# Performance work log

Hardware: AMD Instinct MI355X
Metric: run time of the kernel (lower is better)

Reference implementation:

```python
import jax, jax.numpy as jnp
import numpy as np

B, T, F = 4096, 256, 20
VOCAB, EMB = 1281, 4
UNITS = (64, 32, 32, 32)


def setup_inputs() -> dict:
    key = jax.random.key(0)
    ks = jax.random.split(key, 16)
    feats = jax.random.normal(ks[0], (B, T, F), jnp.float32)
    ids = jax.random.randint(ks[1], (B, T), 0, VOCAB).astype(jnp.float32)
    input_tensor = feats.at[:, :, 1].set(ids)  # column 1 = org ids
    W_emb = jax.random.normal(ks[2], (VOCAB, EMB), jnp.float32) * 0.1
    in_dims = (F - 2 + 1 + EMB,) + UNITS[:-1]  # (23, 64, 32, 32)
    out = {"input_tensor": input_tensor, "W_emb": W_emb}
    for i, (din, u) in enumerate(zip(in_dims, UNITS)):
        out[f"k{i}"] = jax.random.normal(ks[3 + 3 * i], (din, 3 * u), jnp.float32) * 0.1
        out[f"rk{i}"] = jax.random.normal(ks[4 + 3 * i], (u, 3 * u), jnp.float32) * 0.1
        out[f"b{i}"] = jnp.zeros((2, 3 * u), jnp.float32)  # [input_bias, recurrent_bias] (reset_after)
    out["Wd"] = jax.random.normal(ks[15], (UNITS[-1], 2), jnp.float32) * 0.1
    out["bd"] = jnp.zeros((2,), jnp.float32)
    return out


def _gru(h, x, k, rk, b):
    # Keras GRUCell, reset_after=True (TF2 default)
    mx = x @ k + b[0]
    mh = h @ rk + b[1]
    xz, xr, xh = jnp.split(mx, 3, axis=-1)
    hz, hr, hh = jnp.split(mh, 3, axis=-1)
    z = jax.nn.sigmoid(xz + hz)
    r = jax.nn.sigmoid(xr + hr)
    hc = jnp.tanh(xh + r * hh)
    return z * h + (1.0 - z) * hc


def reference(input_tensor, W_emb, k0, rk0, b0, k1, rk1, b1, k2, rk2, b2, k3, rk3, b3, Wd, bd):
    f0 = input_tensor[:, :, :1]                      # [B,T,1]
    ids = input_tensor[:, :, 1].astype(jnp.int32)    # [B,T]
    rest = input_tensor[:, :, 2:]                    # [B,T,F-2]
    emb = W_emb[ids]                                 # [B,T,EMB]
    x = jnp.concatenate([f0, rest, emb], axis=-1)    # [B,T,F+3]
    xs = jnp.swapaxes(x, 0, 1)                       # [T,B,F+3]
    bsz = x.shape[0]
    h_init = tuple(jnp.zeros((bsz, u), x.dtype) for u in UNITS)
    layer_params = ((k0, rk0, b0), (k1, rk1, b1), (k2, rk2, b2), (k3, rk3, b3))

    def step(carry, xt):
        hs = []
        inp = xt
        for h, (k, rk, b) in zip(carry, layer_params):
            h = _gru(h, inp, k, rk, b)
            hs.append(h)
            inp = h
        return tuple(hs), None

    hs, _ = jax.lax.scan(step, h_init, xs)
    # return_sequences + [:, -1, :] == final hidden state of last layer
    logits = hs[-1] @ Wd + bd
    return jax.nn.softmax(logits, axis=-1)
```

## Files before the change

### kernel.cpp

```cpp
#include <hip/hip_runtime.h>


typedef __attribute__((ext_vector_type(8))) __bf16 bf16x8;
typedef __attribute__((ext_vector_type(4))) float f32x4;

#define TT 256
#define FF 20
#define BT 16
#define CH 64
#define SH0 72
#define SH1 40
#define XSTR 648
#define NTHR 768
#define LOG2E 1.44269504f

__device__ __forceinline__ f32x4 mfma16(bf16x8 a, bf16x8 b, f32x4 c) {
  return __builtin_amdgcn_mfma_f32_16x16x32_bf16(a, b, c, 0, 0, 0);
}

__device__ __forceinline__ bf16x8 bfragW(const float* W, int Kreal, int N,
                                         int ncol, int kbase) {
  bf16x8 r;
#pragma unroll
  for (int j = 0; j < 8; ++j) {
    int k = kbase + j;
    r[j] = (__bf16)(k < Kreal ? W[k * N + ncol] : 0.f);
  }
  return r;
}

extern "C" __global__ void __launch_bounds__(NTHR, 3)
gru4(const float* __restrict__ inp, const float* __restrict__ Wemb,
     const float* __restrict__ k0, const float* __restrict__ rk0, const float* __restrict__ b0,
     const float* __restrict__ k1, const float* __restrict__ rk1, const float* __restrict__ b1,
     const float* __restrict__ k2, const float* __restrict__ rk2, const float* __restrict__ b2,
     const float* __restrict__ k3, const float* __restrict__ rk3, const float* __restrict__ b3,
     const float* __restrict__ Wd, const float* __restrict__ bd,
     float* __restrict__ out)
{
  __shared__ __align__(16) __bf16 x_ch[CH * XSTR];
  __shared__ __align__(16) __bf16 h0_lds[2][BT * SH0];
  __shared__ __align__(16) __bf16 h1_lds[2][BT * SH1];
  __shared__ __align__(16) __bf16 h2_lds[2][BT * SH1];
  __shared__ __align__(16) __bf16 h3_lds[2][BT * SH1];
  __shared__ __align__(16) float h3f[BT * 32];

  const int tid  = threadIdx.x;
  const int lane = tid & 63;
  const int w    = tid >> 6;
  const int col  = lane & 15;
  const int kb   = (lane >> 4) * 8;
  const int rowq = (lane >> 4) * 4;
  const long bbase = (long)blockIdx.x * BT;
  const float* binp = inp + bbase * TT * FF;

  bf16x8 zf;
#pragma unroll
  for (int j = 0; j < 8; ++j) zf[j] = (__bf16)0.f;

  bf16x8 WzP = zf, WrP = zf, WgP = zf;
  bf16x8 WzX = zf, WrX = zf, WgX = zf;
  bf16x8 WzO = zf, WrO = zf, WgO = zf;
  float bz = 0.f, br = 0.f, bxh = 0.f, bhh = 0.f;
  const __bf16 *P0b = x_ch, *X1b = x_ch, *O0b = x_ch;
  int DP = 0, DX = 0, DO = 0;
  __bf16* Wwr0 = (__bf16*)h3f;
  int WD = 0, wstride = SH1;
  int lay = 0;
  bool doLo = false, doHi = false, hasX1pre = false, hasX1own = false;

  if (w < 6) {
    lay = 0; hasX1own = true;
    const int sl = (w < 4) ? (w >> 1) : (w - 2);
    doLo = (w >= 4) || ((w & 1) == 0);
    doHi = (w >= 4) || ((w & 1) == 1);
    const int u = sl * 16 + col;
    WzP = bfragW(k0, 23, 192, u, kb);
    WrP = bfragW(k0, 23, 192, 64 + u, kb);
    WgP = bfragW(k0, 23, 192, 128 + u, kb);
    WzO = bfragW(rk0, 64, 192, u, kb);
    WrO = bfragW(rk0, 64, 192, 64 + u, kb);
    WgO = bfragW(rk0, 64, 192, 128 + u, kb);
    WzX = bfragW(rk0, 64, 192, u, 32 + kb);
    WrX = bfragW(rk0, 64, 192, 64 + u, 32 + kb);
    WgX = bfragW(rk0, 64, 192, 128 + u, 32 + kb);
    bz  = b0[u] + b0[192 + u];
    br  = b0[64 + u] + b0[192 + 64 + u];
    bxh = b0[128 + u];
    bhh = b0[192 + 128 + u];
    O0b = &h0_lds[0][col * SH0 + kb];      DO = BT * SH0;
    X1b = &h0_lds[0][col * SH0 + 32 + kb]; DX = BT * SH0;
    Wwr0 = &h0_lds[0][rowq * SH0 + sl * 16 + col];
    WD = BT * SH0; wstride = SH0;
  } else if (w < 8) {
    lay = 1; hasX1pre = true; doLo = doHi = true;
    const int u = (w - 6) * 16 + col;
    WzP = bfragW(k1, 64, 96, u, kb);
    WrP = bfragW(k1, 64, 96, 32 + u, kb);
    WgP = bfragW(k1, 64, 96, 64 + u, kb);
    WzX = bfragW(k1, 64, 96, u, 32 + kb);
    WrX = bfragW(k1, 64, 96, 32 + u, 32 + kb);
    WgX = bfragW(k1, 64, 96, 64 + u, 32 + kb);
    WzO = bfragW(rk1, 32, 96, u, kb);
    WrO = bfragW(rk1, 32, 96, 32 + u, kb);
    WgO = bfragW(rk1, 32, 96, 64 + u, kb);
    bz  = b1[u] + b1[96 + u];
    br  = b1[32 + u] + b1[96 + 32 + u];
    bxh = b1[64 + u];
    bhh = b1[96 + 64 + u];
    P0b = &h0_lds[0][col * SH0 + kb];      DP = BT * SH0;
    X1b = &h0_lds[0][col * SH0 + 32 + kb]; DX = BT * SH0;
    O0b = &h1_lds[0][col * SH1 + kb];      DO = BT * SH1;
    Wwr0 = &h1_lds[0][rowq * SH1 + (w - 6) * 16 + col];
    WD = BT * SH1; wstride = SH1;
  } else if (w < 10) {
    lay = 2; doLo = doHi = true;
    const int u = (w - 8) * 16 + col;
    WzP = bfragW(k2, 32, 96, u, kb);
    WrP = bfragW(k2, 32, 96, 32 + u, kb);
    WgP = bfragW(k2, 32, 96, 64 + u, kb);
    WzO = bfragW(rk2, 32, 96, u, kb);
    WrO = bfragW(rk2, 32, 96, 32 + u, kb);
    WgO = bfragW(rk2, 32, 96, 64 + u, kb);
    bz  = b2[u] + b2[96 + u];
    br  = b2[32 + u] + b2[96 + 32 + u];
    bxh = b2[64 + u];
    bhh = b2[96 + 64 + u];
    P0b = &h1_lds[0][col * SH1 + kb]; DP = BT * SH1;
    O0b = &h2_lds[0][col * SH1 + kb]; DO = BT * SH1;
    Wwr0 = &h2_lds[0][rowq * SH1 + (w - 8) * 16 + col];
    WD = BT * SH1; wstride = SH1;
  } else {
    lay = 3; doLo = doHi = true;
    const int u = (w - 10) * 16 + col;
    WzP = bfragW(k3, 32, 96, u, kb);
    WrP = bfragW(k3, 32, 96, 32 + u, kb);
    WgP = bfragW(k3, 32, 96, 64 + u, kb);
    WzO = bfragW(rk3, 32, 96, u, kb);
    WrO = bfragW(rk3, 32, 96, 32 + u, kb);
    WgO = bfragW(rk3, 32, 96, 64 + u, kb);
    bz  = b3[u] + b3[96 + u];
    br  = b3[32 + u] + b3[96 + 32 + u];
    bxh = b3[64 + u];
    bhh = b3[96 + 64 + u];
    P0b = &h2_lds[0][col * SH1 + kb]; DP = BT * SH1;
    O0b = &h3_lds[0][col * SH1 + kb]; DO = BT * SH1;
    Wwr0 = &h3_lds[0][rowq * SH1 + (w - 10) * 16 + col];
    WD = BT * SH1; wstride = SH1;
  }

  const __bf16* xb = &x_ch[col * 40 + kb];

  {
    __bf16* p0 = (__bf16*)h0_lds;
    for (int i = tid; i < 2 * BT * SH0; i += NTHR) p0[i] = (__bf16)0.f;
    __bf16* p1 = (__bf16*)h1_lds;
    __bf16* p2 = (__bf16*)h2_lds;
    __bf16* p3 = (__bf16*)h3_lds;
    for (int i = tid; i < 2 * BT * SH1; i += NTHR) {
      p1[i] = (__bf16)0.f; p2[i] = (__bf16)0.f; p3[i] = (__bf16)0.f;
    }
  }
  float hreg[4] = {0.f, 0.f, 0.f, 0.f};
  bf16x8 P0 = zf, X1 = zf;
  __syncthreads();

  for (int s = 0; s < TT + 6; ++s) {
    if ((s & (CH - 1)) == 0 && s < TT) {
      for (int idx = tid; idx < BT * CH; idx += NTHR) {
        const int row = idx >> 6;
        const int tg  = idx & (CH - 1);
        const float* p = binp + ((long)row * TT + s + tg) * FF;
        float4 v0 = *(const float4*)(p);
        float4 v1 = *(const float4*)(p + 4);
        float4 v2 = *(const float4*)(p + 8);
        float4 v3 = *(const float4*)(p + 12);
        float4 v4 = *(const float4*)(p + 16);
        float4 e  = *(const float4*)(Wemb + 4 * (int)v0.y);
        __bf16* d = &x_ch[tg * XSTR + row * 40];
        bf16x8 q0 = {(__bf16)v0.x, (__bf16)v0.z, (__bf16)v0.w, (__bf16)v1.x,
                     (__bf16)v1.y, (__bf16)v1.z, (__bf16)v1.w, (__bf16)v2.x};
        bf16x8 q1 = {(__bf16)v2.y, (__bf16)v2.z, (__bf16)v2.w, (__bf16)v3.x,
                     (__bf16)v3.y, (__bf16)v3.z, (__bf16)v3.w, (__bf16)v4.x};
        bf16x8 q2 = {(__bf16)v4.y, (__bf16)v4.z, (__bf16)v4.w, (__bf16)e.x,
                     (__bf16)e.y,  (__bf16)e.z,  (__bf16)e.w,  (__bf16)0.f};
        *(bf16x8*)(d)      = q0;
        *(bf16x8*)(d + 8)  = q1;
        *(bf16x8*)(d + 16) = q2;
        *(bf16x8*)(d + 24) = zf;
      }
      __syncthreads();
      if (lay == 0) P0 = *(const bf16x8*)(xb);
    }

    const int pb = (s + 1) & 1;
    const int qb = s & 1;
    const int t  = s - 2 * lay;
    const bool active = (t >= 0) && (t < TT);

    f32x4 az, ar, axh, ahh;
    bf16x8 O0;
    if (active) {
      O0 = *(const bf16x8*)(O0b + pb * DO);
      if (hasX1own) X1 = *(const bf16x8*)(X1b + pb * DX);
      az  = f32x4{bz, bz, bz, bz};
      ar  = f32x4{br, br, br, br};
      axh = f32x4{bxh, bxh, bxh, bxh};
      ahh = f32x4{bhh, bhh, bhh, bhh};
      az  = mfma16(P0, WzP, az);
      ar  = mfma16(P0, WrP, ar);
      axh = mfma16(P0, WgP, axh);
      if (hasX1pre) {
        az  = mfma16(X1, WzX, az);
        ar  = mfma16(X1, WrX, ar);
        axh = mfma16(X1, WgX, axh);
      }
      az  = mfma16(O0, WzO, az);
      ar  = mfma16(O0, WrO, ar);
      ahh = mfma16(O0, WgO, ahh);
      if (hasX1own) {
        az  = mfma16(X1, WzX, az);
        ar  = mfma16(X1, WrX, ar);
        ahh = mfma16(X1, WgX, ahh);
      }
    }

    const int tn = t + 1;
    if (tn >= 0 && tn < TT) {
      if (lay == 0) {
        const int pl = (s + 1) & (CH - 1);
        if (pl != 0) P0 = *(const bf16x8*)(xb + pl * XSTR);
      } else {
        P0 = *(const bf16x8*)(P0b + pb * DP);
        if (hasX1pre) X1 = *(const bf16x8*)(X1b + pb * DX);
      }
    }

    if (active) {
      __bf16* wr = Wwr0 + qb * WD;
#define GATE(r) { \
        float yz = fminf(fmaxf(az[r], -44.f), 44.f) * -LOG2E; \
        float yr = fminf(fmaxf(ar[r], -44.f), 44.f) * -LOG2E; \
        float Ez = __builtin_amdgcn_exp2f(yz); \
        float Er = __builtin_amdgcn_exp2f(yr); \
        float dz = 1.f + Ez, dr = 1.f + Er; \
        float inv = __builtin_amdgcn_rcpf(dz * dr); \
        float z  = inv * dr; \
        float rg = inv * dz; \
        float uu = fmaf(rg, ahh[r], axh[r]); \
        float Eg = __builtin_amdgcn_exp2f(uu * (-2.f * LOG2E)); \
        float hc = fmaf(2.f, __builtin_amdgcn_rcpf(1.f + Eg), -1.f); \
        float hn = fmaf(z, hreg[r] - hc, hc); \
        hreg[r] = hn; \
        wr[(r) * wstride] = (__bf16)hn; }

      if (doLo) { GATE(0); GATE(1); }
      if (doHi) { GATE(2); GATE(3); }
#undef GATE
    }

    __syncthreads();
  }

  if (w >= 10) {
#pragma unroll
    for (int r = 0; r < 4; ++r)
      h3f[(rowq + r) * 32 + (w - 10) * 16 + col] = hreg[r];
  }
  __syncthreads();

  if (tid < BT) {
    float l0 = bd[0], l1 = bd[1];
#pragma unroll
    for (int u = 0; u < 32; ++u) {
      float h = h3f[tid * 32 + u];
      l0 = fmaf(h, Wd[2 * u], l0);
      l1 = fmaf(h, Wd[2 * u + 1], l1);
    }
    float m = fmaxf(l0, l1);
    float e0 = __builtin_amdgcn_exp2f((l0 - m) * LOG2E);
    float e1 = __builtin_amdgcn_exp2f((l1 - m) * LOG2E);
    float inv = 1.f / (e0 + e1);
    out[(bbase + tid) * 2 + 0] = e0 * inv;
    out[(bbase + tid) * 2 + 1] = e1 * inv;
  }
}

extern "C" void kernel_launch(void* const* d_in, const int* in_sizes, int n_in,
                              void* d_out, int out_size, void* d_ws, size_t ws_size,
                              hipStream_t stream) {
  const float* inp  = (const float*)d_in[0];
  const float* Wemb = (const float*)d_in[1];
  const float* k0   = (const float*)d_in[2];
  const float* rk0  = (const float*)d_in[3];
  const float* b0   = (const float*)d_in[4];
  const float* k1   = (const float*)d_in[5];
  const float* rk1  = (const float*)d_in[6];
  const float* b1   = (const float*)d_in[7];
  const float* k2   = (const float*)d_in[8];
  const float* rk2  = (const float*)d_in[9];
  const float* b2   = (const float*)d_in[10];
  const float* k3   = (const float*)d_in[11];
  const float* rk3  = (const float*)d_in[12];
  const float* b3   = (const float*)d_in[13];
  const float* Wd   = (const float*)d_in[14];
  const float* bd   = (const float*)d_in[15];
  float* out = (float*)d_out;

  const int Btot = in_sizes[0] / (TT * FF);
  dim3 grid(Btot / BT);
  gru4<<<grid, NTHR, 0, stream>>>(inp, Wemb, k0, rk0, b0, k1, rk1, b1,
                                  k2, rk2, b2, k3, rk3, b3, Wd, bd, out);
}
```

Measured before the change: 367.8 us.

## Replace per-step block barriers with flag-based wavefront pipelining and loader warps

Drops the per-timestep __syncthreads in favour of LDS flag counters. Each layer's waves spin-wait only on their own producer, consumer and peer waves, and hidden states are kept in an 8-deep ring so layers can run several steps apart. Two dedicated waves stream the input through a double-buffered 16-step x ring, which removes the chunked block-wide load stalls. The layer-0 work split changes from six waves to four, and layer 2/3 now use two waves each. The risks are spin-wait overhead, memory-ordering correctness relying on threadfence_block with volatile flags, and more LDS use.

```diff
diff --git a/kernel.cpp b/kernel.cpp
--- a/kernel.cpp
+++ b/kernel.cpp
@@ -7,10 +7,14 @@
 #define TT 256
 #define FF 20
 #define BT 16
-#define CH 64
-#define SH0 72
-#define SH1 40
-#define XSTR 648
+#define XCH 16
+#define NXS 2
+#define XROW 40
+#define XPLANE (BT * XROW)
+#define XSLOT (XCH * XPLANE)
+#define H0S 72
+#define H1S 40
+#define RD 8
 #define NTHR 768
 #define LOG2E 1.44269504f
 
@@ -28,6 +32,8 @@
   }
   return r;
 }
+
+__device__ __forceinline__ int imin(int a, int b) { return a < b ? a : b; }
 
 extern "C" __global__ void __launch_bounds__(NTHR, 3)
 gru4(const float* __restrict__ inp, const float* __restrict__ Wemb,
@@ -38,12 +44,13 @@
      const float* __restrict__ Wd, const float* __restrict__ bd,
      float* __restrict__ out)
 {
-  __shared__ __align__(16) __bf16 x_ch[CH * XSTR];
-  __shared__ __align__(16) __bf16 h0_lds[2][BT * SH0];
-  __shared__ __align__(16) __bf16 h1_lds[2][BT * SH1];
-  __shared__ __align__(16) __bf16 h2_lds[2][BT * SH1];
-  __shared__ __align__(16) __bf16 h3_lds[2][BT * SH1];
+  __shared__ __align__(16) __bf16 x_ring[NXS * XSLOT];
+  __shared__ __align__(16) __bf16 h0ring[RD * BT * H0S];
+  __shared__ __align__(16) __bf16 h1ring[RD * BT * H1S];
+  __shared__ __align__(16) __bf16 h2ring[RD * BT * H1S];
+  __shared__ __align__(16) __bf16 h3ring[RD * BT * H1S];
   __shared__ __align__(16) float h3f[BT * 32];
+  __shared__ int flg[16];
 
   const int tid  = threadIdx.x;
   const int lane = tid & 63;
@@ -58,126 +65,41 @@
 #pragma unroll
   for (int j = 0; j < 8; ++j) zf[j] = (__bf16)0.f;
 
-  bf16x8 WzP = zf, WrP = zf, WgP = zf;
-  bf16x8 WzX = zf, WrX = zf, WgX = zf;
-  bf16x8 WzO = zf, WrO = zf, WgO = zf;
-  float bz = 0.f, br = 0.f, bxh = 0.f, bhh = 0.f;
-  const __bf16 *P0b = x_ch, *X1b = x_ch, *O0b = x_ch;
-  int DP = 0, DX = 0, DO = 0;
-  __bf16* Wwr0 = (__bf16*)h3f;
-  int WD = 0, wstride = SH1;
-  int lay = 0;
-  bool doLo = false, doHi = false, hasX1pre = false, hasX1own = false;
-
-  if (w < 6) {
-    lay = 0; hasX1own = true;
-    const int sl = (w < 4) ? (w >> 1) : (w - 2);
-    doLo = (w >= 4) || ((w & 1) == 0);
-    doHi = (w >= 4) || ((w & 1) == 1);
-    const int u = sl * 16 + col;
-    WzP = bfragW(k0, 23, 192, u, kb);
-    WrP = bfragW(k0, 23, 192, 64 + u, kb);
-    WgP = bfragW(k0, 23, 192, 128 + u, kb);
-    WzO = bfragW(rk0, 64, 192, u, kb);
-    WrO = bfragW(rk0, 64, 192, 64 + u, kb);
-    WgO = bfragW(rk0, 64, 192, 128 + u, kb);
-    WzX = bfragW(rk0, 64, 192, u, 32 + kb);
-    WrX = bfragW(rk0, 64, 192, 64 + u, 32 + kb);
-    WgX = bfragW(rk0, 64, 192, 128 + u, 32 + kb);
-    bz  = b0[u] + b0[192 + u];
-    br  = b0[64 + u] + b0[192 + 64 + u];
-    bxh = b0[128 + u];
-    bhh = b0[192 + 128 + u];
-    O0b = &h0_lds[0][col * SH0 + kb];      DO = BT * SH0;
-    X1b = &h0_lds[0][col * SH0 + 32 + kb]; DX = BT * SH0;
-    Wwr0 = &h0_lds[0][rowq * SH0 + sl * 16 + col];
-    WD = BT * SH0; wstride = SH0;
-  } else if (w < 8) {
-    lay = 1; hasX1pre = true; doLo = doHi = true;
-    const int u = (w - 6) * 16 + col;
-    WzP = bfragW(k1, 64, 96, u, kb);
-    WrP = bfragW(k1, 64, 96, 32 + u, kb);
-    WgP = bfragW(k1, 64, 96, 64 + u, kb);
-    WzX = bfragW(k1, 64, 96, u, 32 + kb);
-    WrX = bfragW(k1, 64, 96, 32 + u, 32 + kb);
-    WgX = bfragW(k1, 64, 96, 64 + u, 32 + kb);
-    WzO = bfragW(rk1, 32, 96, u, kb);
-    WrO = bfragW(rk1, 32, 96, 32 + u, kb);
-    WgO = bfragW(rk1, 32, 96, 64 + u, kb);
-    bz  = b1[u] + b1[96 + u];
-    br  = b1[32 + u] + b1[96 + 32 + u];
-    bxh = b1[64 + u];
-    bhh = b1[96 + 64 + u];
-    P0b = &h0_lds[0][col * SH0 + kb];      DP = BT * SH0;
-    X1b = &h0_lds[0][col * SH0 + 32 + kb]; DX = BT * SH0;
-    O0b = &h1_lds[0][col * SH1 + kb];      DO = BT * SH1;
-    Wwr0 = &h1_lds[0][rowq * SH1 + (w - 6) * 16 + col];
-    WD = BT * SH1; wstride = SH1;
-  } else if (w < 10) {
-    lay = 2; doLo = doHi = true;
-    const int u = (w - 8) * 16 + col;
-    WzP = bfragW(k2, 32, 96, u, kb);
-    WrP = bfragW(k2, 32, 96, 32 + u, kb);
-    WgP = bfragW(k2, 32, 96, 64 + u, kb);
-    WzO = bfragW(rk2, 32, 96, u, kb);
-    WrO = bfragW(rk2, 32, 96, 32 + u, kb);
-    WgO = bfragW(rk2, 32, 96, 64 + u, kb);
-    bz  = b2[u] + b2[96 + u];
-    br  = b2[32 + u] + b2[96 + 32 + u];
-    bxh = b2[64 + u];
-    bhh = b2[96 + 64 + u];
-    P0b = &h1_lds[0][col * SH1 + kb]; DP = BT * SH1;
-    O0b = &h2_lds[0][col * SH1 + kb]; DO = BT * SH1;
-    Wwr0 = &h2_lds[0][rowq * SH1 + (w - 8) * 16 + col];
-    WD = BT * SH1; wstride = SH1;
-  } else {
-    lay = 3; doLo = doHi = true;
-    const int u = (w - 10) * 16 + col;
-    WzP = bfragW(k3, 32, 96, u, kb);
-    WrP = bfragW(k3, 32, 96, 32 + u, kb);
-    WgP = bfragW(k3, 32, 96, 64 + u, kb);
-    WzO = bfragW(rk3, 32, 96, u, kb);
-    WrO = bfragW(rk3, 32, 96, 32 + u, kb);
-    WgO = bfragW(rk3, 32, 96, 64 + u, kb);
-    bz  = b3[u] + b3[96 + u];
-    br  = b3[32 + u] + b3[96 + 32 + u];
-    bxh = b3[64 + u];
-    bhh = b3[96 + 64 + u];
-    P0b = &h2_lds[0][col * SH1 + kb]; DP = BT * SH1;
-    O0b = &h3_lds[0][col * SH1 + kb]; DO = BT * SH1;
-    Wwr0 = &h3_lds[0][rowq * SH1 + (w - 10) * 16 + col];
-    WD = BT * SH1; wstride = SH1;
+  for (int i = tid; i < RD * BT * H0S; i += NTHR) h0ring[i] = (__bf16)0.f;
+  for (int i = tid; i < RD * BT * H1S; i += NTHR) {
+    h1ring[i] = (__bf16)0.f; h2ring[i] = (__bf16)0.f; h3ring[i] = (__bf16)0.f;
   }
-
-  const __bf16* xb = &x_ch[col * 40 + kb];
-
-  {
-    __bf16* p0 = (__bf16*)h0_lds;
-    for (int i = tid; i < 2 * BT * SH0; i += NTHR) p0[i] = (__bf16)0.f;
-    __bf16* p1 = (__bf16*)h1_lds;
-    __bf16* p2 = (__bf16*)h2_lds;
-    __bf16* p3 = (__bf16*)h3_lds;
-    for (int i = tid; i < 2 * BT * SH1; i += NTHR) {
-      p1[i] = (__bf16)0.f; p2[i] = (__bf16)0.f; p3[i] = (__bf16)0.f;
-    }
-  }
-  float hreg[4] = {0.f, 0.f, 0.f, 0.f};
-  bf16x8 P0 = zf, X1 = zf;
+  if (tid < 16) flg[tid] = -1;
   __syncthreads();
 
-  for (int s = 0; s < TT + 6; ++s) {
-    if ((s & (CH - 1)) == 0 && s < TT) {
-      for (int idx = tid; idx < BT * CH; idx += NTHR) {
-        const int row = idx >> 6;
-        const int tg  = idx & (CH - 1);
-        const float* p = binp + ((long)row * TT + s + tg) * FF;
+  volatile int* vf = flg;
+
+  if (w >= 10) {
+    const int sid = w - 10;
+    const int r0 = sid * 8;
+    for (int c = 0; c < TT / XCH; ++c) {
+      if (c >= NXS) {
+        const int need = XCH * (c - (NXS - 1));
+        for (;;) {
+          int m = imin(imin(vf[0], vf[1]), imin(vf[2], vf[3]));
+          if (m >= need) break;
+          __builtin_amdgcn_s_sleep(1);
+        }
+      }
+      __bf16* xs = &x_ring[(c & (NXS - 1)) * XSLOT];
+#pragma unroll
+      for (int k = 0; k < 2; ++k) {
+        const int task = k * 64 + lane;
+        const int row = r0 + (task >> 4);
+        const int tt  = task & 15;
+        const float* p = binp + ((long)row * TT + c * XCH + tt) * FF;
         float4 v0 = *(const float4*)(p);
         float4 v1 = *(const float4*)(p + 4);
         float4 v2 = *(const float4*)(p + 8);
         float4 v3 = *(const float4*)(p + 12);
         float4 v4 = *(const float4*)(p + 16);
         float4 e  = *(const float4*)(Wemb + 4 * (int)v0.y);
-        __bf16* d = &x_ch[tg * XSTR + row * 40];
+        __bf16* d = xs + tt * XPLANE + row * XROW;
         bf16x8 q0 = {(__bf16)v0.x, (__bf16)v0.z, (__bf16)v0.w, (__bf16)v1.x,
                      (__bf16)v1.y, (__bf16)v1.z, (__bf16)v1.w, (__bf16)v2.x};
         bf16x8 q1 = {(__bf16)v2.y, (__bf16)v2.z, (__bf16)v2.w, (__bf16)v3.x,
@@ -189,55 +111,145 @@
         *(bf16x8*)(d + 16) = q2;
         *(bf16x8*)(d + 24) = zf;
       }
-      __syncthreads();
-      if (lay == 0) P0 = *(const bf16x8*)(xb);
-    }
-
-    const int pb = (s + 1) & 1;
-    const int qb = s & 1;
-    const int t  = s - 2 * lay;
-    const bool active = (t >= 0) && (t < TT);
-
-    f32x4 az, ar, axh, ahh;
-    bf16x8 O0;
-    if (active) {
-      O0 = *(const bf16x8*)(O0b + pb * DO);
-      if (hasX1own) X1 = *(const bf16x8*)(X1b + pb * DX);
-      az  = f32x4{bz, bz, bz, bz};
-      ar  = f32x4{br, br, br, br};
-      axh = f32x4{bxh, bxh, bxh, bxh};
-      ahh = f32x4{bhh, bhh, bhh, bhh};
-      az  = mfma16(P0, WzP, az);
-      ar  = mfma16(P0, WrP, ar);
-      axh = mfma16(P0, WgP, axh);
-      if (hasX1pre) {
-        az  = mfma16(X1, WzX, az);
-        ar  = mfma16(X1, WrX, ar);
-        axh = mfma16(X1, WgX, axh);
+      __threadfence_block();
+      if (lane == 0) vf[10 + sid] = c;
+    }
+  } else {
+    int role, half;
+    if (w < 4)      { role = 0; half = w; }
+    else if (w < 6) { role = 2; half = w - 4; }
+    else if (w < 8) { role = 1; half = w - 6; }
+    else            { role = 3; half = w - 8; }
+    const int uc = half * 16 + col;
+
+    bf16x8 Wz0, Wz1, Wz2 = zf, Wr0, Wr1, Wr2 = zf, Wg0, Wg1, Wg2 = zf;
+    float bz, br, bxh, bhh;
+    const __bf16 *a0b = x_ring, *a1b = h0ring, *a2b = h0ring;
+    int s0 = 0, s1 = 0, s2 = 0;
+    __bf16* wb; int wS, wSlot;
+    bool hasA2, g1in, isL0;
+    int oB, oC, iB, iC, pB = 0, pC, myIdx;
+
+    if (role == 0) {
+      isL0 = true; hasA2 = true; g1in = false;
+      Wz0 = bfragW(k0, 23, 192, uc, kb);
+      Wz1 = bfragW(rk0, 64, 192, uc, kb);
+      Wz2 = bfragW(rk0, 64, 192, uc, 32 + kb);
+      Wr0 = bfragW(k0, 23, 192, 64 + uc, kb);
+      Wr1 = bfragW(rk0, 64, 192, 64 + uc, kb);
+      Wr2 = bfragW(rk0, 64, 192, 64 + uc, 32 + kb);
+      Wg0 = bfragW(k0, 23, 192, 128 + uc, kb);
+      Wg1 = bfragW(rk0, 64, 192, 128 + uc, kb);
+      Wg2 = bfragW(rk0, 64, 192, 128 + uc, 32 + kb);
+      bz  = b0[uc] + b0[192 + uc];
+      br  = b0[64 + uc] + b0[192 + 64 + uc];
+      bxh = b0[128 + uc];
+      bhh = b0[192 + 128 + uc];
+      a0b = &x_ring[col * XROW + kb];
+      a1b = &h0ring[col * H0S + kb];      s1 = BT * H0S;
+      a2b = &h0ring[col * H0S + 32 + kb]; s2 = BT * H0S;
+      wb = &h0ring[rowq * H0S + uc]; wS = H0S; wSlot = BT * H0S;
+      oB = 0; oC = 4; iB = 10; iC = 2; pB = 4; pC = 2; myIdx = half;
+    } else if (role == 1) {
+      isL0 = false; hasA2 = true; g1in = true;
+      Wz0 = bfragW(k1, 64, 96, uc, kb);
+      Wz1 = bfragW(k1, 64, 96, uc, 32 + kb);
+      Wz2 = bfragW(rk1, 32, 96, uc, kb);
+      Wr0 = bfragW(k1, 64, 96, 32 + uc, kb);
+      Wr1 = bfragW(k1, 64, 96, 32 + uc, 32 + kb);
+      Wr2 = bfragW(rk1, 32, 96, 32 + uc, kb);
+      Wg0 = bfragW(k1, 64, 96, 64 + uc, kb);
+      Wg1 = bfragW(k1, 64, 96, 64 + uc, 32 + kb);
+      Wg2 = bfragW(rk1, 32, 96, 64 + uc, kb);
+      bz  = b1[uc] + b1[96 + uc];
+      br  = b1[32 + uc] + b1[96 + 32 + uc];
+      bxh = b1[64 + uc];
+      bhh = b1[96 + 64 + uc];
+      a0b = &h0ring[col * H0S + kb];      s0 = BT * H0S;
+      a1b = &h0ring[col * H0S + 32 + kb]; s1 = BT * H0S;
+      a2b = &h1ring[col * H1S + kb];      s2 = BT * H1S;
+      wb = &h1ring[rowq * H1S + uc]; wS = H1S; wSlot = BT * H1S;
+      oB = 4; oC = 2; iB = 0; iC = 4; pB = 6; pC = 2; myIdx = 4 + half;
+    } else if (role == 2) {
+      isL0 = false; hasA2 = false; g1in = false;
+      Wz0 = bfragW(k2, 32, 96, uc, kb);
+      Wz1 = bfragW(rk2, 32, 96, uc, kb);
+      Wr0 = bfragW(k2, 32, 96, 32 + uc, kb);
+      Wr1 = bfragW(rk2, 32, 96, 32 + uc, kb);
+      Wg0 = bfragW(k2, 32, 96, 64 + uc, kb);
+      Wg1 = bfragW(rk2, 32, 96, 64 + uc, kb);
+      bz  = b2[uc] + b2[96 + uc];
+      br  = b2[32 + uc] + b2[96 + 32 + uc];
+      bxh = b2[64 + uc];
+      bhh = b2[96 + 64 + uc];
+      a0b = &h1ring[col * H1S + kb]; s0 = BT * H1S;
+      a1b = &h2ring[col * H1S + kb]; s1 = BT * H1S;
+      wb = &h2ring[rowq * H1S + uc]; wS = H1S; wSlot = BT * H1S;
+      oB = 6; oC = 2; iB = 4; iC = 2; pB = 8; pC = 2; myIdx = 6 + half;
+    } else {
+      isL0 = false; hasA2 = false; g1in = false;
+      Wz0 = bfragW(k3, 32, 96, uc, kb);
+      Wz1 = bfragW(rk3, 32, 96, uc, kb);
+      Wr0 = bfragW(k3, 32, 96, 32 + uc, kb);
+      Wr1 = bfragW(rk3, 32, 96, 32 + uc, kb);
+      Wg0 = bfragW(k3, 32, 96, 64 + uc, kb);
+      Wg1 = bfragW(rk3, 32, 96, 64 + uc, kb);
+      bz  = b3[uc] + b3[96 + uc];
+      br  = b3[32 + uc] + b3[96 + 32 + uc];
+      bxh = b3[64 + uc];
+      bhh = b3[96 + 64 + uc];
+      a0b = &h2ring[col * H1S + kb]; s0 = BT * H1S;
+      a1b = &h3ring[col * H1S + kb]; s1 = BT * H1S;
+      wb = &h3ring[rowq * H1S + uc]; wS = H1S; wSlot = BT * H1S;
+      oB = 8; oC = 2; iB = 6; iC = 2; pC = 0; myIdx = 8 + half;
+    }
+    const bool a1prev = (role != 1);
+
+    float hreg[4] = {0.f, 0.f, 0.f, 0.f};
+
+    for (int t = 0; t < TT; ++t) {
+      const int inNeed = isL0 ? (t >> 4) : t;
+      for (;;) {
+        int m = imin(vf[oB], vf[oB + 1]);
+        if (oC == 4) m = imin(m, imin(vf[oB + 2], vf[oB + 3]));
+        int mi = imin(vf[iB], vf[iB + 1]);
+        if (iC == 4) mi = imin(mi, imin(vf[iB + 2], vf[iB + 3]));
+        bool ok = (m >= t - 1) && (mi >= inNeed);
+        if (pC) ok = ok && (imin(vf[pB], vf[pB + 1]) >= t - RD);
+        if (ok) break;
+        __builtin_amdgcn_s_sleep(1);
       }
-      az  = mfma16(O0, WzO, az);
-      ar  = mfma16(O0, WrO, ar);
-      ahh = mfma16(O0, WgO, ahh);
-      if (hasX1own) {
-        az  = mfma16(X1, WzX, az);
-        ar  = mfma16(X1, WrX, ar);
-        ahh = mfma16(X1, WgX, ahh);
+      __threadfence_block();
+
+      const int sPrev = (t - 1) & (RD - 1);
+      const int sCur  = t & (RD - 1);
+      bf16x8 A0, A1, A2 = zf;
+      if (isL0)
+        A0 = *(const bf16x8*)(a0b + ((t >> 4) & (NXS - 1)) * XSLOT
+                                  + (t & (XCH - 1)) * XPLANE);
+      else
+        A0 = *(const bf16x8*)(a0b + sCur * s0);
+      A1 = *(const bf16x8*)(a1b + (a1prev ? sPrev : sCur) * s1);
+      if (hasA2) A2 = *(const bf16x8*)(a2b + sPrev * s2);
+
+      f32x4 az  = {bz, bz, bz, bz};
+      f32x4 ar  = {br, br, br, br};
+      f32x4 axh = {bxh, bxh, bxh, bxh};
+      f32x4 ahh = {bhh, bhh, bhh, bhh};
+      az = mfma16(A0, Wz0, az);
+      ar = mfma16(A0, Wr0, ar);
+      axh = mfma16(A0, Wg0, axh);
+      az = mfma16(A1, Wz1, az);
+      ar = mfma16(A1, Wr1, ar);
+      if (g1in) axh = mfma16(A1, Wg1, axh);
+      else      ahh = mfma16(A1, Wg1, ahh);
+      if (hasA2) {
+        az = mfma16(A2, Wz2, az);
+        ar = mfma16(A2, Wr2, ar);
+        ahh = mfma16(A2, Wg2, ahh);
       }
-    }
-
-    const int tn = t + 1;
-    if (tn >= 0 && tn < TT) {
-      if (lay == 0) {
-        const int pl = (s + 1) & (CH - 1);
-        if (pl != 0) P0 = *(const bf16x8*)(xb + pl * XSTR);
-      } else {
-        P0 = *(const bf16x8*)(P0b + pb * DP);
-        if (hasX1pre) X1 = *(const bf16x8*)(X1b + pb * DX);
-      }
-    }
-
-    if (active) {
-      __bf16* wr = Wwr0 + qb * WD;
+
+      __bf16* wr = wb + sCur * wSlot;
 #define GATE(r) { \
         float yz = fminf(fmaxf(az[r], -44.f), 44.f) * -LOG2E; \
         float yr = fminf(fmaxf(ar[r], -44.f), 44.f) * -LOG2E; \
@@ -252,21 +264,21 @@
         float hc = fmaf(2.f, __builtin_amdgcn_rcpf(1.f + Eg), -1.f); \
         float hn = fmaf(z, hreg[r] - hc, hc); \
         hreg[r] = hn; \
-        wr[(r) * wstride] = (__bf16)hn; }
-
-      if (doLo) { GATE(0); GATE(1); }
-      if (doHi) { GATE(2); GATE(3); }
+        wr[(r) * wS] = (__bf16)hn; }
+      GATE(0); GATE(1); GATE(2); GATE(3);
 #undef GATE
-    }
-
-    __syncthreads();
+
+      __threadfence_block();
+      if (lane == 0) vf[myIdx] = t;
+    }
+
+    if (role == 3) {
+#pragma unroll
+      for (int r = 0; r < 4; ++r)
+        h3f[(rowq + r) * 32 + uc] = hreg[r];
+    }
   }
 
-  if (w >= 10) {
-#pragma unroll
-    for (int r = 0; r < 4; ++r)
-      h3f[(rowq + r) * 32 + (w - 10) * 16 + col] = hreg[r];
-  }
   __syncthreads();
 
   if (tid < BT) {
```

New measurement: 405.9 us. +10.4%, slower.
